# Optimization experiments

Measured on AMD Instinct MI355X. Metric: run time of the kernel, lower is better.

## Reference

```python
import jax, jax.numpy as jnp
import numpy as np

EMBED = 768
HEADS = 12


def setup_inputs() -> dict:
    key = jax.random.key(0)
    k1, k2, k3, k4, k5 = jax.random.split(key, 5)
    B, N, E = 8, 1024, EMBED
    x = jax.random.normal(k1, (B, N, E), dtype=jnp.float32)
    # torch Linear stored as [in, out] here (math-equivalent: y = x @ W + b)
    w_qkv = jax.random.normal(k2, (E, 3 * E), dtype=jnp.float32) * (E ** -0.5)
    b_qkv = jax.random.normal(k3, (3 * E,), dtype=jnp.float32) * 0.02
    w_proj = jax.random.normal(k4, (E, E), dtype=jnp.float32) * (E ** -0.5)
    b_proj = jax.random.normal(k5, (E,), dtype=jnp.float32) * 0.02
    return {"x": x, "w_qkv": w_qkv, "b_qkv": b_qkv, "w_proj": w_proj, "b_proj": b_proj}


def reference(x, w_qkv, b_qkv, w_proj, b_proj):
    B, N, E = x.shape
    H = HEADS
    D = E // H
    qkv = x @ w_qkv + b_qkv                       # [B, N, 3E]
    # rearrange 'b n (h d qkv) -> qkv b h n d': qkv index is innermost in last dim
    qkv = qkv.reshape(B, N, H, D, 3)
    qkv = jnp.transpose(qkv, (4, 0, 2, 1, 3))      # [3, B, H, N, D]
    q, k, v = qkv[0], qkv[1], qkv[2]
    energy = jnp.einsum('bhqd,bhkd->bhqk', q, k)   # [B, H, N, N]
    scaling = float(E) ** 0.5
    # NOTE: original scales AFTER softmax (unusual but faithful)
    att = jax.nn.softmax(energy, axis=-1) / scaling
    # dropout_prob = 0.0 -> identity
    out = jnp.einsum('bhqk,bhkd->bhqd', att, v)    # [B, H, N, D]
    out = jnp.transpose(out, (0, 2, 1, 3)).reshape(B, N, E)
    return out @ w_proj + b_proj
```

## Files before the change

### kernel.cpp

```cpp
#include <hip/hip_runtime.h>
#include <hip/hip_bf16.h>
#include <stdint.h>

#define NSEQ 1024
#define EMB 768
#define HEADS 12
#define HD 64
#define BATCH 8
#define BHN (BATCH*HEADS)

typedef __attribute__((ext_vector_type(8))) short bf16x8;
typedef __attribute__((ext_vector_type(4))) short bf16x4;
typedef __attribute__((ext_vector_type(4))) float f32x4;

typedef const void __attribute__((address_space(1))) cglobal_void;
typedef void __attribute__((address_space(3))) lds_void_t;

#define LOG2E 1.4426950408889634f

__device__ __forceinline__ void load_lds16(const void* g, void* l) {
    __builtin_amdgcn_global_load_lds((cglobal_void*)g, (lds_void_t*)l, 16, 0, 0);
}

__device__ __forceinline__ unsigned short f2bf(float f) {
    __hip_bfloat16 h = __float2bfloat16(f);
    return *reinterpret_cast<unsigned short*>(&h);
}

__device__ __forceinline__ float exp2_hw(float x) {
#if __has_builtin(__builtin_amdgcn_exp2f)
    return __builtin_amdgcn_exp2f(x);
#else
    return exp2f(x);
#endif
}

__global__ void conv_x_kernel(const float* __restrict__ x, unsigned short* __restrict__ xb) {
    int i = (blockIdx.x * 256 + threadIdx.x) * 4;
    float4 v = *reinterpret_cast<const float4*>(x + i);
    ushort4 o;
    o.x = f2bf(v.x); o.y = f2bf(v.y); o.z = f2bf(v.z); o.w = f2bf(v.w);
    *reinterpret_cast<ushort4*>(xb + i) = o;
}

template <int PERM>
__global__ void transpose_w_kernel(const float* __restrict__ w, unsigned short* __restrict__ wt,
                                   int K, int C) {
    __shared__ unsigned short tile[64][65];
    int c0 = blockIdx.x * 64;
    int k0 = blockIdx.y * 64;
    int t = threadIdx.x;
    int r = t >> 2, cc = (t & 3) * 16;
#pragma unroll
    for (int e = 0; e < 16; e += 4) {
        float4 v = *reinterpret_cast<const float4*>(w + (size_t)(k0 + r) * C + c0 + cc + e);
        float s0 = (PERM && ((c0 + cc + e + 0) % 3 == 0)) ? LOG2E : 1.0f;
        float s1 = (PERM && ((c0 + cc + e + 1) % 3 == 0)) ? LOG2E : 1.0f;
        float s2 = (PERM && ((c0 + cc + e + 2) % 3 == 0)) ? LOG2E : 1.0f;
        float s3 = (PERM && ((c0 + cc + e + 3) % 3 == 0)) ? LOG2E : 1.0f;
        tile[r][cc + e + 0] = f2bf(v.x * s0);
        tile[r][cc + e + 1] = f2bf(v.y * s1);
        tile[r][cc + e + 2] = f2bf(v.z * s2);
        tile[r][cc + e + 3] = f2bf(v.w * s3);
    }
    __syncthreads();
    int c = t >> 2, kk0 = (t & 3) * 16;
    int cg = c0 + c;
    int n;
    if (PERM) {
        int qkv = cg % 3, h = cg / 192, d = (cg % 192) / 3;
        n = qkv * EMB + h * HD + d;
    } else {
        n = cg;
    }
    uint4 lo, hi;
    lo.x = (unsigned)tile[kk0 + 0][c] | ((unsigned)tile[kk0 + 1][c] << 16);
    lo.y = (unsigned)tile[kk0 + 2][c] | ((unsigned)tile[kk0 + 3][c] << 16);
    lo.z = (unsigned)tile[kk0 + 4][c] | ((unsigned)tile[kk0 + 5][c] << 16);
    lo.w = (unsigned)tile[kk0 + 6][c] | ((unsigned)tile[kk0 + 7][c] << 16);
    hi.x = (unsigned)tile[kk0 + 8][c] | ((unsigned)tile[kk0 + 9][c] << 16);
    hi.y = (unsigned)tile[kk0 + 10][c] | ((unsigned)tile[kk0 + 11][c] << 16);
    hi.z = (unsigned)tile[kk0 + 12][c] | ((unsigned)tile[kk0 + 13][c] << 16);
    hi.w = (unsigned)tile[kk0 + 14][c] | ((unsigned)tile[kk0 + 15][c] << 16);
    *reinterpret_cast<uint4*>(wt + (size_t)n * K + k0 + kk0) = lo;
    *reinterpret_cast<uint4*>(wt + (size_t)n * K + k0 + kk0 + 8) = hi;
}

__global__ void perm_bias_kernel(const float* __restrict__ b, float* __restrict__ bp) {
    int c = blockIdx.x * 256 + threadIdx.x;
    int qkv = c % 3, h = c / 192, d = (c % 192) / 3;
    bp[qkv * EMB + h * HD + d] = (qkv == 0) ? b[c] * LOG2E : b[c];
}

template <int MODE>
__launch_bounds__(256, 2)
__global__ void gemm_bt_kernel(const unsigned short* __restrict__ A,
                               const unsigned short* __restrict__ Bt,
                               const float* __restrict__ bias,
                               float* __restrict__ out,
                               unsigned short* __restrict__ qout,
                               unsigned short* __restrict__ kout,
                               unsigned short* __restrict__ vout,
                               int M, int N, int K, int tiles_n) {
    __shared__ unsigned short lds_a[128 * 64];
    __shared__ unsigned short lds_b[128 * 64];
    int bx = blockIdx.x;
    int tm = bx / tiles_n, tn = bx % tiles_n;
    int m0 = tm * 128, n0 = tn * 128;
    int t = threadIdx.x;
    int l = t & 63;
    int wr = (t >> 7) & 1, wc = (t >> 6) & 1;
    int wbase = (t & 192);

    f32x4 acc[4][4];
#pragma unroll
    for (int i = 0; i < 4; i++)
#pragma unroll
        for (int j = 0; j < 4; j++)
#pragma unroll
            for (int r = 0; r < 4; r++) acc[i][j][r] = 0.f;

    for (int kt = 0; kt < K; kt += 64) {
        __syncthreads();
#pragma unroll
        for (int i = 0; i < 4; i++) {
            int c = i * 256 + t;
            int row = c >> 3;
            int sc = ((c & 7) ^ (row & 7)) * 8;
            load_lds16(A + (size_t)(m0 + row) * K + kt + sc, lds_a + (size_t)(i * 256 + wbase) * 8);
            load_lds16(Bt + (size_t)(n0 + row) * K + kt + sc, lds_b + (size_t)(i * 256 + wbase) * 8);
        }
        __syncthreads();
#pragma unroll
        for (int kk = 0; kk < 2; kk++) {
            int cb = kk * 64 + (l >> 4) * 16;
            bf16x8 af[4], bfr[4];
#pragma unroll
            for (int i = 0; i < 4; i++) {
                int row = wr * 64 + i * 16 + (l & 15);
                af[i] = *reinterpret_cast<const bf16x8*>(
                    (const char*)lds_a + row * 128 + (cb ^ ((row & 7) << 4)));
            }
#pragma unroll
            for (int j = 0; j < 4; j++) {
                int row = wc * 64 + j * 16 + (l & 15);
                bfr[j] = *reinterpret_cast<const bf16x8*>(
                    (const char*)lds_b + row * 128 + (cb ^ ((row & 7) << 4)));
            }
#pragma unroll
            for (int i = 0; i < 4; i++)
#pragma unroll
                for (int j = 0; j < 4; j++) {
                    if (MODE == 2)
                        acc[i][j] = __builtin_amdgcn_mfma_f32_16x16x32_bf16(bfr[j], af[i], acc[i][j], 0, 0, 0);
                    else
                        acc[i][j] = __builtin_amdgcn_mfma_f32_16x16x32_bf16(af[i], bfr[j], acc[i][j], 0, 0, 0);
                }
        }
    }

    if (MODE == 2) {
#pragma unroll
        for (int j = 0; j < 4; j++) {
#pragma unroll
            for (int r = 0; r < 4; r++) {
                int nv = wc * 64 + j * 16 + ((l >> 4) * 4) + r + n0;
                float bv = bias[nv];
                int hh = nv >> 6, dd = nv & 63;
#pragma unroll
                for (int i = 0; i < 4; i++) {
                    int m_g = m0 + wr * 64 + i * 16 + (l & 15);
                    int bb = m_g >> 10, nn = m_g & 1023;
                    int nnp = (nn & ~31) | ((nn & 12) << 1) | ((nn >> 2) & 4) | (nn & 3);
                    vout[((size_t)(bb * HEADS + hh) * HD + dd) * NSEQ + nnp] =
                        f2bf(acc[i][j][r] + bv);
                }
            }
        }
    } else {
#pragma unroll
        for (int i = 0; i < 4; i++) {
            int mbase = m0 + wr * 64 + i * 16 + ((l >> 4) * 4);
#pragma unroll
            for (int j = 0; j < 4; j++) {
                int n_g = n0 + wc * 64 + j * 16 + (l & 15);
                float bv = bias[n_g];
#pragma unroll
                for (int r = 0; r < 4; r++) {
                    int m_g = mbase + r;
                    float v = acc[i][j][r] + bv;
                    if (MODE == 0) {
                        int rem = n_g - ((n_g >= 768) ? 768 : 0);
                        int hh = rem >> 6, dd = rem & 63;
                        int bb = m_g >> 10, nn = m_g & 1023;
                        if (n_g < 768)
                            qout[(size_t)((bb * HEADS + hh) * NSEQ + nn) * HD + dd] = f2bf(v);
                        else
                            kout[(size_t)((bb * HEADS + hh) * NSEQ + nn) * HD + dd] = f2bf(v);
                    } else {
                        out[(size_t)m_g * N + n_g] = v;
                    }
                }
            }
        }
    }
}

__launch_bounds__(512, 8)
__global__ void attn_kernel(const unsigned short* __restrict__ Q,
                            const unsigned short* __restrict__ K,
                            const unsigned short* __restrict__ Vt,
                            unsigned short* __restrict__ Oout) {
    __shared__ unsigned short k_lds[2][64 * 64];
    __shared__ unsigned short vt_lds[2][64 * 64];
    int bx = blockIdx.x;
    int bh = bx % BHN;
    int q0 = (bx / BHN) << 7;
    int b = bh / HEADS, h = bh % HEADS;
    int t = threadIdx.x, w = t >> 6, l = t & 63;
    int g = l >> 4, c16 = l & 15;
    const unsigned short* Qh = Q + (size_t)bh * NSEQ * HD;
    const unsigned short* Kh = K + (size_t)bh * NSEQ * HD;
    const unsigned short* Vth = Vt + (size_t)bh * NSEQ * HD;

    int qr = q0 + w * 16 + c16;
    bf16x8 qf[2];
    qf[0] = *reinterpret_cast<const bf16x8*>(Qh + (size_t)qr * HD + g * 8);
    qf[1] = *reinterpret_cast<const bf16x8*>(Qh + (size_t)qr * HD + 32 + g * 8);

    float l_run = 0.f;
    f32x4 acc[4];
#pragma unroll
    for (int jd = 0; jd < 4; jd++)
#pragma unroll
        for (int r = 0; r < 4; r++) acc[jd][r] = 0.f;

    auto stage = [&](int buf, int kv) {
        int row = t >> 3;
        int sc = ((t & 7) ^ (row & 7)) * 8;
        load_lds16(Kh + (size_t)(kv + row) * HD + sc, k_lds[buf] + (size_t)(t & ~63) * 8);
        load_lds16(Vth + (size_t)row * NSEQ + kv + sc, vt_lds[buf] + (size_t)(t & ~63) * 8);
    };

    stage(0, 0);
    __syncthreads();
    int cur = 0;
    for (int it = 0; it < 16; ++it) {
        if (it < 15) stage(cur ^ 1, (it + 1) << 6);

        const char* kbase = (const char*)k_lds[cur];
        const char* vbase = (const char*)vt_lds[cur];

        f32x4 st[4];
#pragma unroll
        for (int jk = 0; jk < 4; jk++)
#pragma unroll
            for (int r = 0; r < 4; r++) st[jk][r] = 0.f;
        __builtin_amdgcn_s_setprio(1);
#pragma unroll
        for (int kk = 0; kk < 2; kk++) {
            int cb = kk * 64 + g * 16;
#pragma unroll
            for (int jk = 0; jk < 4; jk++) {
                int row = jk * 16 + c16;
                bf16x8 kf = *reinterpret_cast<const bf16x8*>(
                    kbase + row * 128 + (cb ^ ((row & 7) << 4)));
                st[jk] = __builtin_amdgcn_mfma_f32_16x16x32_bf16(kf, qf[kk], st[jk], 0, 0, 0);
            }
        }
        __builtin_amdgcn_s_setprio(0);

#pragma unroll
        for (int jk = 0; jk < 4; jk++)
#pragma unroll
            for (int r = 0; r < 4; r++) st[jk][r] = exp2_hw(st[jk][r]);

        bf16x8 pf0, pf1;
#pragma unroll
        for (int r = 0; r < 4; r++) { pf0[r] = (short)f2bf(st[0][r]); pf0[4 + r] = (short)f2bf(st[1][r]); }
#pragma unroll
        for (int r = 0; r < 4; r++) { pf1[r] = (short)f2bf(st[2][r]); pf1[4 + r] = (short)f2bf(st[3][r]); }

        __builtin_amdgcn_s_setprio(1);
#pragma unroll
        for (int ks = 0; ks < 2; ks++) {
            bf16x8 pf = ks ? pf1 : pf0;
            int cb = ks * 64 + g * 16;
#pragma unroll
            for (int jd = 0; jd < 4; jd++) {
                int row = jd * 16 + c16;
                bf16x8 vf = *reinterpret_cast<const bf16x8*>(
                    vbase + row * 128 + (cb ^ ((row & 7) << 4)));
                acc[jd] = __builtin_amdgcn_mfma_f32_16x16x32_bf16(vf, pf, acc[jd], 0, 0, 0);
            }
        }
        __builtin_amdgcn_s_setprio(0);

        float ps = (((st[0][0] + st[0][1]) + (st[0][2] + st[0][3])) +
                    ((st[1][0] + st[1][1]) + (st[1][2] + st[1][3]))) +
                   (((st[2][0] + st[2][1]) + (st[2][2] + st[2][3])) +
                    ((st[3][0] + st[3][1]) + (st[3][2] + st[3][3])));
        ps += __shfl_xor(ps, 16);
        ps += __shfl_xor(ps, 32);
        l_run += ps;

        __syncthreads();
        cur ^= 1;
    }

    const float scale = 27.712812921102035f;
    float inv = 1.0f / (l_run * scale);
    size_t qbase = ((size_t)(b * NSEQ + qr) * HEADS + h) * HD;
#pragma unroll
    for (int jd = 0; jd < 4; jd++)
#pragma unroll
        for (int r = 0; r < 4; r++) {
            int d = jd * 16 + g * 4 + r;
            Oout[qbase + d] = f2bf(acc[jd][r] * inv);
        }
}

extern "C" void kernel_launch(void* const* d_in, const int* in_sizes, int n_in,
                              void* d_out, int out_size, void* d_ws, size_t ws_size,
                              hipStream_t stream) {
    const float* x = (const float*)d_in[0];
    const float* w_qkv = (const float*)d_in[1];
    const float* b_qkv = (const float*)d_in[2];
    const float* w_proj = (const float*)d_in[3];
    const float* b_proj = (const float*)d_in[4];

    char* ws = (char*)d_ws;
    unsigned short* xb      = (unsigned short*)(ws + 0);
    unsigned short* wt_qkv  = (unsigned short*)(ws + 12582912);
    unsigned short* wt_proj = (unsigned short*)(ws + 16121856);
    float*          biasp   = (float*)(ws + 17301504);
    unsigned short* qb      = (unsigned short*)(ws + 17310720);
    unsigned short* kb      = (unsigned short*)(ws + 29893632);
    unsigned short* vtb     = (unsigned short*)(ws + 42476544);
    unsigned short* ao      = (unsigned short*)(ws + 55059456);

    conv_x_kernel<<<6144, 256, 0, stream>>>(x, xb);
    transpose_w_kernel<1><<<dim3(36, 12), 256, 0, stream>>>(w_qkv, wt_qkv, EMB, 3 * EMB);
    transpose_w_kernel<0><<<dim3(12, 12), 256, 0, stream>>>(w_proj, wt_proj, EMB, EMB);
    perm_bias_kernel<<<9, 256, 0, stream>>>(b_qkv, biasp);

    gemm_bt_kernel<0><<<64 * 12, 256, 0, stream>>>(xb, wt_qkv, biasp, nullptr, qb, kb, nullptr,
                                                   8192, 3 * EMB, EMB, 12);
    gemm_bt_kernel<2><<<64 * 6, 256, 0, stream>>>(xb, wt_qkv + (size_t)1536 * EMB, biasp + 1536,
                                                  nullptr, nullptr, nullptr, vtb,
                                                  8192, 3 * EMB, EMB, 6);
    attn_kernel<<<BHN * 8, 512, 0, stream>>>(qb, kb, vtb, ao);
    gemm_bt_kernel<1><<<64 * 6, 256, 0, stream>>>(ao, wt_proj, b_proj, (float*)d_out,
                                                  nullptr, nullptr, nullptr,
                                                  8192, EMB, EMB, 6);
}
```

Before: 116.5 us.

## Process two query row tiles per wave in attention kernel, halving block size

Each wave in the attention kernel now handles 32 query rows as two 16-row tiles, so every K and V fragment read from LDS feeds two MFMAs instead of one. Blocks shrink from 512 to 256 threads while still covering 128 query rows, and each thread issues two LDS-staging loads per buffer. The aim is to halve LDS read traffic per MFMA and raise MFMA density. The cost is roughly double the accumulator and score registers per thread, which may lower occupancy; the launch bounds change reflects that.

```diff
diff --git a/kernel.cpp b/kernel.cpp
--- a/kernel.cpp
+++ b/kernel.cpp
@@ -206,7 +206,7 @@
     }
 }
 
-__launch_bounds__(512, 8)
+__launch_bounds__(256, 3)
 __global__ void attn_kernel(const unsigned short* __restrict__ Q,
                             const unsigned short* __restrict__ K,
                             const unsigned short* __restrict__ Vt,
@@ -223,23 +223,30 @@
     const unsigned short* Kh = K + (size_t)bh * NSEQ * HD;
     const unsigned short* Vth = Vt + (size_t)bh * NSEQ * HD;
 
-    int qr = q0 + w * 16 + c16;
-    bf16x8 qf[2];
-    qf[0] = *reinterpret_cast<const bf16x8*>(Qh + (size_t)qr * HD + g * 8);
-    qf[1] = *reinterpret_cast<const bf16x8*>(Qh + (size_t)qr * HD + 32 + g * 8);
-
-    float l_run = 0.f;
-    f32x4 acc[4];
+    int qrA = q0 + w * 32 + c16;
+    int qrB = qrA + 16;
+    bf16x8 qfA[2], qfB[2];
+    qfA[0] = *reinterpret_cast<const bf16x8*>(Qh + (size_t)qrA * HD + g * 8);
+    qfA[1] = *reinterpret_cast<const bf16x8*>(Qh + (size_t)qrA * HD + 32 + g * 8);
+    qfB[0] = *reinterpret_cast<const bf16x8*>(Qh + (size_t)qrB * HD + g * 8);
+    qfB[1] = *reinterpret_cast<const bf16x8*>(Qh + (size_t)qrB * HD + 32 + g * 8);
+
+    float lA = 0.f, lB = 0.f;
+    f32x4 accA[4], accB[4];
 #pragma unroll
     for (int jd = 0; jd < 4; jd++)
 #pragma unroll
-        for (int r = 0; r < 4; r++) acc[jd][r] = 0.f;
+        for (int r = 0; r < 4; r++) { accA[jd][r] = 0.f; accB[jd][r] = 0.f; }
 
     auto stage = [&](int buf, int kv) {
-        int row = t >> 3;
-        int sc = ((t & 7) ^ (row & 7)) * 8;
-        load_lds16(Kh + (size_t)(kv + row) * HD + sc, k_lds[buf] + (size_t)(t & ~63) * 8);
-        load_lds16(Vth + (size_t)row * NSEQ + kv + sc, vt_lds[buf] + (size_t)(t & ~63) * 8);
+#pragma unroll
+        for (int i = 0; i < 2; i++) {
+            int tt = i * 256 + t;
+            int row = tt >> 3;
+            int sc = ((tt & 7) ^ (row & 7)) * 8;
+            load_lds16(Kh + (size_t)(kv + row) * HD + sc, k_lds[buf] + (size_t)(tt & ~63) * 8);
+            load_lds16(Vth + (size_t)row * NSEQ + kv + sc, vt_lds[buf] + (size_t)(tt & ~63) * 8);
+        }
     };
 
     stage(0, 0);
@@ -251,11 +258,11 @@
         const char* kbase = (const char*)k_lds[cur];
         const char* vbase = (const char*)vt_lds[cur];
 
-        f32x4 st[4];
+        f32x4 stA[4], stB[4];
 #pragma unroll
         for (int jk = 0; jk < 4; jk++)
 #pragma unroll
-            for (int r = 0; r < 4; r++) st[jk][r] = 0.f;
+            for (int r = 0; r < 4; r++) { stA[jk][r] = 0.f; stB[jk][r] = 0.f; }
         __builtin_amdgcn_s_setprio(1);
 #pragma unroll
         for (int kk = 0; kk < 2; kk++) {
@@ -265,7 +272,8 @@
                 int row = jk * 16 + c16;
                 bf16x8 kf = *reinterpret_cast<const bf16x8*>(
                     kbase + row * 128 + (cb ^ ((row & 7) << 4)));
-                st[jk] = __builtin_amdgcn_mfma_f32_16x16x32_bf16(kf, qf[kk], st[jk], 0, 0, 0);
+                stA[jk] = __builtin_amdgcn_mfma_f32_16x16x32_bf16(kf, qfA[kk], stA[jk], 0, 0, 0);
+                stB[jk] = __builtin_amdgcn_mfma_f32_16x16x32_bf16(kf, qfB[kk], stB[jk], 0, 0, 0);
             }
         }
         __builtin_amdgcn_s_setprio(0);
@@ -273,50 +281,66 @@
 #pragma unroll
         for (int jk = 0; jk < 4; jk++)
 #pragma unroll
-            for (int r = 0; r < 4; r++) st[jk][r] = exp2_hw(st[jk][r]);
-
-        bf16x8 pf0, pf1;
-#pragma unroll
-        for (int r = 0; r < 4; r++) { pf0[r] = (short)f2bf(st[0][r]); pf0[4 + r] = (short)f2bf(st[1][r]); }
-#pragma unroll
-        for (int r = 0; r < 4; r++) { pf1[r] = (short)f2bf(st[2][r]); pf1[4 + r] = (short)f2bf(st[3][r]); }
+            for (int r = 0; r < 4; r++) {
+                stA[jk][r] = exp2_hw(stA[jk][r]);
+                stB[jk][r] = exp2_hw(stB[jk][r]);
+            }
+
+        bf16x8 pfA[2], pfB[2];
+#pragma unroll
+        for (int r = 0; r < 4; r++) {
+            pfA[0][r] = (short)f2bf(stA[0][r]); pfA[0][4 + r] = (short)f2bf(stA[1][r]);
+            pfA[1][r] = (short)f2bf(stA[2][r]); pfA[1][4 + r] = (short)f2bf(stA[3][r]);
+            pfB[0][r] = (short)f2bf(stB[0][r]); pfB[0][4 + r] = (short)f2bf(stB[1][r]);
+            pfB[1][r] = (short)f2bf(stB[2][r]); pfB[1][4 + r] = (short)f2bf(stB[3][r]);
+        }
 
         __builtin_amdgcn_s_setprio(1);
 #pragma unroll
         for (int ks = 0; ks < 2; ks++) {
-            bf16x8 pf = ks ? pf1 : pf0;
             int cb = ks * 64 + g * 16;
 #pragma unroll
             for (int jd = 0; jd < 4; jd++) {
                 int row = jd * 16 + c16;
                 bf16x8 vf = *reinterpret_cast<const bf16x8*>(
                     vbase + row * 128 + (cb ^ ((row & 7) << 4)));
-                acc[jd] = __builtin_amdgcn_mfma_f32_16x16x32_bf16(vf, pf, acc[jd], 0, 0, 0);
+                accA[jd] = __builtin_amdgcn_mfma_f32_16x16x32_bf16(vf, pfA[ks], accA[jd], 0, 0, 0);
+                accB[jd] = __builtin_amdgcn_mfma_f32_16x16x32_bf16(vf, pfB[ks], accB[jd], 0, 0, 0);
             }
         }
         __builtin_amdgcn_s_setprio(0);
 
-        float ps = (((st[0][0] + st[0][1]) + (st[0][2] + st[0][3])) +
-                    ((st[1][0] + st[1][1]) + (st[1][2] + st[1][3]))) +
-                   (((st[2][0] + st[2][1]) + (st[2][2] + st[2][3])) +
-                    ((st[3][0] + st[3][1]) + (st[3][2] + st[3][3])));
-        ps += __shfl_xor(ps, 16);
-        ps += __shfl_xor(ps, 32);
-        l_run += ps;
+        float psA = (((stA[0][0] + stA[0][1]) + (stA[0][2] + stA[0][3])) +
+                     ((stA[1][0] + stA[1][1]) + (stA[1][2] + stA[1][3]))) +
+                    (((stA[2][0] + stA[2][1]) + (stA[2][2] + stA[2][3])) +
+                     ((stA[3][0] + stA[3][1]) + (stA[3][2] + stA[3][3])));
+        float psB = (((stB[0][0] + stB[0][1]) + (stB[0][2] + stB[0][3])) +
+                     ((stB[1][0] + stB[1][1]) + (stB[1][2] + stB[1][3]))) +
+                    (((stB[2][0] + stB[2][1]) + (stB[2][2] + stB[2][3])) +
+                     ((stB[3][0] + stB[3][1]) + (stB[3][2] + stB[3][3])));
+        psA += __shfl_xor(psA, 16);
+        psA += __shfl_xor(psA, 32);
+        psB += __shfl_xor(psB, 16);
+        psB += __shfl_xor(psB, 32);
+        lA += psA;
+        lB += psB;
 
         __syncthreads();
         cur ^= 1;
     }
 
     const float scale = 27.712812921102035f;
-    float inv = 1.0f / (l_run * scale);
-    size_t qbase = ((size_t)(b * NSEQ + qr) * HEADS + h) * HD;
+    float invA = 1.0f / (lA * scale);
+    float invB = 1.0f / (lB * scale);
+    size_t qbaseA = ((size_t)(b * NSEQ + qrA) * HEADS + h) * HD;
+    size_t qbaseB = ((size_t)(b * NSEQ + qrB) * HEADS + h) * HD;
 #pragma unroll
     for (int jd = 0; jd < 4; jd++)
 #pragma unroll
         for (int r = 0; r < 4; r++) {
             int d = jd * 16 + g * 4 + r;
-            Oout[qbase + d] = f2bf(acc[jd][r] * inv);
+            Oout[qbaseA + d] = f2bf(accA[jd][r] * invA);
+            Oout[qbaseB + d] = f2bf(accB[jd][r] * invB);
         }
 }
 
@@ -349,7 +373,7 @@
     gemm_bt_kernel<2><<<64 * 6, 256, 0, stream>>>(xb, wt_qkv + (size_t)1536 * EMB, biasp + 1536,
                                                   nullptr, nullptr, nullptr, vtb,
                                                   8192, 3 * EMB, EMB, 6);
-    attn_kernel<<<BHN * 8, 512, 0, stream>>>(qb, kb, vtb, ao);
+    attn_kernel<<<BHN * 8, 256, 0, stream>>>(qb, kb, vtb, ao);
     gemm_bt_kernel<1><<<64 * 6, 256, 0, stream>>>(ao, wt_proj, b_proj, (float*)d_out,
                                                   nullptr, nullptr, nullptr,
                                                   8192, EMB, EMB, 6);
```

Measured after the change: 114.2 us. 1.02x faster.
